# Optimization experiments

Hardware: AMD Instinct MI355X
Metric: run time of the kernel (lower is better)

Reference implementation:

```python
import jax, jax.numpy as jnp
import numpy as np

SIMPLE_W = 1.0
NON_SIMPLE_W = 5.0

# connectivity offset sets (exclude center)
_ALL26 = [(a, b, c) for a in (-1, 0, 1) for b in (-1, 0, 1) for c in (-1, 0, 1) if (a, b, c) != (0, 0, 0)]
OFF6 = [o for o in _ALL26 if abs(o[0]) + abs(o[1]) + abs(o[2]) == 1]          # scipy default structure
OFF18 = [o for o in _ALL26 if not (abs(o[0]) == 1 and abs(o[1]) == 1 and abs(o[2]) == 1)]  # the 's' structure
OFF26 = _ALL26                                                                  # np.ones((3,3,3))


def global_label(fg):
    """Connected-component labels (6-connectivity) via max-propagation.
    Labels are distinct positive ints per component (values differ from scipy's
    1..K but only label *equality* is used downstream). fg: bool [D,H,W]."""
    D, H, W = fg.shape
    idx = (jnp.arange(fg.size, dtype=jnp.int32) + 1).reshape(fg.shape)
    lab0 = jnp.where(fg, idx, 0)

    def step(lab):
        p = jnp.pad(lab, 1)
        m = lab
        for dz, dy, dx in OFF6:
            m = jnp.maximum(m, p[1 + dz:1 + dz + D, 1 + dy:1 + dy + H, 1 + dx:1 + dx + W])
        return jnp.where(fg, m, 0)

    def cond(c):
        return ~c[1]

    def body(c):
        lab, _ = c
        new = step(lab)
        return new, jnp.all(new == lab)

    lab, _ = jax.lax.while_loop(cond, body, (lab0, jnp.array(False)))
    return lab


def local_ncomp(mask, offsets):
    """Number of connected components inside each 3x3x3 window.
    mask: bool [N,3,3,3]. Max-propagation of unique seeds for 26 iters
    (>= max path length among 27 voxels); a component is counted where the
    surviving max label equals its own seed."""
    seed = (jnp.arange(27, dtype=jnp.int32) + 1).reshape(3, 3, 3)
    lab0 = jnp.where(mask, seed, 0)

    def body(_, lab):
        p = jnp.pad(lab, ((0, 0), (1, 1), (1, 1), (1, 1)))
        m = lab
        for dz, dy, dx in offsets:
            m = jnp.maximum(m, p[:, 1 + dz:4 + dz, 1 + dy:4 + dy, 1 + dx:4 + dx])
        return jnp.where(mask, m, 0)

    lab = jax.lax.fori_loop(0, 26, body, lab0)
    return jnp.sum((lab == seed) & mask, axis=(1, 2, 3))


def nonsimple_map(x):
    """Per-voxel non-simple-point indicator, float, same shape as x."""
    D, H, W = x.shape
    fg = x > 0
    glab = global_label(fg)
    p = jnp.pad(glab, 1, mode='edge')  # np.pad(..., 'edge')
    # 3x3x3 label windows per voxel -> [N,3,3,3]
    wins = jnp.stack([p[dz:dz + D, dy:dy + H, dx:dx + W]
                      for dz in range(3) for dy in range(3) for dx in range(3)], axis=-1)
    wins = wins.reshape(-1, 3, 3, 3)
    center = wins[:, 1, 1, 1]  # [N]
    c = center[:, None, None, None]
    # test 1: complement-of-center-label components (18-connectivity) must be exactly 1
    n1 = local_ncomp(wins != c, OFF18)
    # test 2: center-label components with center voxel removed (26-conn) must be exactly 1
    mask2 = (wins == c).at[:, 1, 1, 1].set(False)
    n2 = local_ncomp(mask2, OFF26)
    ns = (center != 0) & ((n1 != 1) | (n2 != 1))
    return ns.reshape(D, H, W).astype(x.dtype)


def setup_inputs() -> dict:
    key = jax.random.key(0)
    k1, k2 = jax.random.split(key)
    D = H = W = 64
    prediction = jax.random.normal(k1, (D, H, W), dtype=jnp.float32)
    label = jax.random.randint(k2, (D, H, W), 0, 2).astype(jnp.float32)
    return {"prediction": prediction, "label": label}


def reference(prediction, label):
    pw = nonsimple_map(prediction)
    lw = nonsimple_map(label)
    w_bool = (pw + lw) > 0
    weight = jnp.where(w_bool, NON_SIMPLE_W, SIMPLE_W).astype(prediction.dtype)
    # BCEWithLogitsLoss(reduction='none'): max(x,0) - x*y + log(1+exp(-|x|))
    cost = jnp.maximum(prediction, 0.0) - prediction * label + jnp.log1p(jnp.exp(-jnp.abs(prediction)))
    return jnp.mean(weight * cost)
```

## Files before the change

### kernel.cpp

```cpp
#include <hip/hip_runtime.h>

#define DIM 64
#define NVOX (DIM * DIM * DIM)

__device__ __forceinline__ int find_root_link(int* L, int v) {
    for (;;) {
        int p = L[v];
        if (p == v) return v;
        int gp = L[p];
        if (gp == p) return p;
        L[v] = gp;
        v = gp;
    }
}

__device__ __forceinline__ void unite(int* L, int a, int b) {
    int ra = find_root_link(L, a);
    int rb = find_root_link(L, b);
    while (ra != rb) {
        if (ra > rb) { int t = ra; ra = rb; rb = t; }
        int old = atomicCAS(&L[rb], rb, ra);
        if (old == rb) break;
        rb = find_root_link(L, old);
        ra = find_root_link(L, ra);
    }
}

__global__ void local_ccl(const float* __restrict__ pred,
                          const float* __restrict__ lab,
                          int* __restrict__ LP, int* __restrict__ LL) {
    __shared__ int s_lab[2048];
    int t = threadIdx.x;
    int b = blockIdx.x;
    int tx = b & 3, ty = (b >> 2) & 3, tz = b >> 4;
    int X0 = tx << 4, Y0 = ty << 4, Z0 = tz << 3;

    const float* src = blockIdx.y ? lab : pred;
    int* Lg = blockIdx.y ? LL : LP;

    bool fg[8];
    int vv[8];
#pragma unroll
    for (int i = 0; i < 8; ++i) {
        int l = t + (i << 8);
        int v = ((Z0 + (l >> 8)) << 12) | ((Y0 + ((l >> 4) & 15)) << 6)
              | (X0 + (l & 15));
        vv[i] = v;
        fg[i] = src[v] > 0.0f;
        s_lab[l] = fg[i] ? l : -1;
    }
    __syncthreads();

#pragma unroll
    for (int i = 0; i < 8; ++i) {
        if (!fg[i]) continue;
        int l = t + (i << 8);
        int lx = l & 15, ly = (l >> 4) & 15, lz = l >> 8;
        if (lx < 15 && s_lab[l + 1]   >= 0) unite(s_lab, l, l + 1);
        if (ly < 15 && s_lab[l + 16]  >= 0) unite(s_lab, l, l + 16);
        if (lz < 7  && s_lab[l + 256] >= 0) unite(s_lab, l, l + 256);
    }
    __syncthreads();

#pragma unroll
    for (int i = 0; i < 8; ++i) {
        int g = -1;
        if (fg[i]) {
            int p = s_lab[t + (i << 8)];
            while (s_lab[p] != p) p = s_lab[p];
            g = ((Z0 + (p >> 8)) << 12) | ((Y0 + ((p >> 4) & 15)) << 6)
              | (X0 + (p & 15));
        }
        Lg[vv[i]] = g;
    }
}

#define EPF 53248

__global__ void boundary_link(int* __restrict__ LP, int* __restrict__ LL) {
    int e = blockIdx.x * blockDim.x + threadIdx.x;
    int f = e >= EPF;
    int r = f ? e - EPF : e;
    int* L = f ? LL : LP;
    int v, n;
    if (r < 12288) {
        int plane = 15 + ((r >> 12) << 4);
        int ij = r & 4095;
        v = ((ij >> 6) << 12) | ((ij & 63) << 6) | plane;
        n = v + 1;
    } else if (r < 24576) {
        int r2 = r - 12288;
        int plane = 15 + ((r2 >> 12) << 4);
        int ij = r2 & 4095;
        v = ((ij >> 6) << 12) | (plane << 6) | (ij & 63);
        n = v + 64;
    } else {
        int r3 = r - 24576;
        int plane = 7 + ((r3 >> 12) << 3);
        int ij = r3 & 4095;
        v = (plane << 12) | ((ij >> 6) << 6) | (ij & 63);
        n = v + 4096;
    }
    if (L[v] >= 0 && L[n] >= 0) unite(L, v, n);
}

#define MX_L 0x6DB6DB6u
#define MX_R 0x36DB6DBu
#define MY_L 0x7E3F1F8u
#define MY_R 0x0FC7E3Fu
#define M27  0x7FFFFFFu

__device__ __forceinline__ unsigned dil26(unsigned m) {
    m |= ((m << 1) & MX_L) | ((m >> 1) & MX_R);
    m |= ((m << 3) & MY_L) | ((m >> 3) & MY_R);
    m |= ((m << 9) & M27)  | (m >> 9);
    return m;
}
__device__ __forceinline__ unsigned dil18(unsigned m) {
    unsigned ax = m | ((m << 1) & MX_L) | ((m >> 1) & MX_R);
    unsigned ay = m | ((m << 3) & MY_L) | ((m >> 3) & MY_R);
    unsigned dxy = ax | ((ax << 3) & MY_L) | ((ax >> 3) & MY_R);
    unsigned dxz = ax | ((ax << 9) & M27)  | (ax >> 9);
    unsigned dyz = ay | ((ay << 9) & M27)  | (ay >> 9);
    return dxy | dxz | dyz;
}

__device__ __forceinline__ bool single18(unsigned m) {
    if (!m) return false;
    unsigned c = m & (~m + 1u);
    for (;;) {
        unsigned n = dil18(c) & m;
        if (n == m) return true;
        if (n == c) return false;
        c = n;
    }
}
__device__ __forceinline__ bool single26(unsigned m) {
    if (!m) return false;
    unsigned c = m & (~m + 1u);
    for (;;) {
        unsigned n = dil26(c) & m;
        if (n == m) return true;
        if (n == c) return false;
        c = n;
    }
}

#define HV 600

__global__ void finalize_kernel(const float* __restrict__ pred,
                                const float* __restrict__ lab,
                                const int* __restrict__ LP,
                                const int* __restrict__ LL,
                                float* __restrict__ out) {
    __shared__ int sP[HV], sL[HV];
    __shared__ float s_part[4];
    int t = threadIdx.x;
    int b = blockIdx.x;
    int tx = b & 7, ty = (b >> 3) & 7, tz = b >> 6;
    int x0 = tx << 3, y0 = ty << 3, z0 = tz << 2;

    for (int i = t; i < HV; i += 256) {
        int hx = i % 10, r = i / 10, hy = r % 10, hz = r / 10;
        int gx = x0 + hx - 1; gx = gx < 0 ? 0 : (gx > 63 ? 63 : gx);
        int gy = y0 + hy - 1; gy = gy < 0 ? 0 : (gy > 63 ? 63 : gy);
        int gz = z0 + hz - 1; gz = gz < 0 ? 0 : (gz > 63 ? 63 : gz);
        int gv = (gz << 12) | (gy << 6) | gx;
        int p = LP[gv];
        if (p >= 0) { int q = LP[p]; while (q != p) { p = q; q = LP[p]; } }
        sP[i] = p;
        p = LL[gv];
        if (p >= 0) { int q = LL[p]; while (q != p) { p = q; q = LL[p]; } }
        sL[i] = p;
    }
    __syncthreads();

    int lx = t & 7, ly = (t >> 3) & 7, lz = t >> 6;
    int x = x0 | lx, y = y0 | ly, z = z0 | lz;
    int v = (z << 12) | (y << 6) | x;
    int base = lz * 100 + ly * 10 + lx;

    bool nsP = false, nsL = false;
    {
        int c = sP[base + 111];
        if (c >= 0) {
            unsigned m1 = 0, m2 = 0; int k = 0;
#pragma unroll
            for (int kz = 0; kz < 3; ++kz)
#pragma unroll
                for (int ky = 0; ky < 3; ++ky)
#pragma unroll
                    for (int kx = 0; kx < 3; ++kx, ++k) {
                        int w = sP[base + kz * 100 + ky * 10 + kx];
                        m1 |= (unsigned)(w != c) << k;
                        m2 |= (unsigned)(w == c) << k;
                    }
            m2 &= ~(1u << 13);
            nsP = !(single18(m1) && single26(m2));
        }
    }
    {
        int c = sL[base + 111];
        if (c >= 0) {
            unsigned m1 = 0, m2 = 0; int k = 0;
#pragma unroll
            for (int kz = 0; kz < 3; ++kz)
#pragma unroll
                for (int ky = 0; ky < 3; ++ky)
#pragma unroll
                    for (int kx = 0; kx < 3; ++kx, ++k) {
                        int w = sL[base + kz * 100 + ky * 10 + kx];
                        m1 |= (unsigned)(w != c) << k;
                        m2 |= (unsigned)(w == c) << k;
                    }
            m2 &= ~(1u << 13);
            nsL = !(single18(m1) && single26(m2));
        }
    }

    float p = pred[v], l = lab[v];
    float cost = fmaxf(p, 0.0f) - p * l + log1pf(__expf(-fabsf(p)));
    float w = (nsP || nsL) ? 5.0f : 1.0f;
    float contrib = w * cost;

#pragma unroll
    for (int off = 32; off > 0; off >>= 1)
        contrib += __shfl_down(contrib, off, 64);
    if ((t & 63) == 0) s_part[t >> 6] = contrib;
    __syncthreads();
    if (t == 0) {
        float s = s_part[0] + s_part[1] + s_part[2] + s_part[3];
        atomicAdd(out, s * (1.0f / (float)NVOX));
    }
}

extern "C" void kernel_launch(void* const* d_in, const int* in_sizes, int n_in,
                              void* d_out, int out_size, void* d_ws, size_t ws_size,
                              hipStream_t stream) {
    const float* pred = (const float*)d_in[0];
    const float* lab  = (const float*)d_in[1];
    float* out = (float*)d_out;

    int* LP = (int*)d_ws;
    int* LL = LP + NVOX;

    hipMemsetAsync(d_out, 0, sizeof(float), stream);

    hipLaunchKernelGGL(local_ccl, dim3(128, 2), dim3(256), 0, stream,
                       pred, lab, LP, LL);
    hipLaunchKernelGGL(boundary_link, dim3(2 * EPF / 256), dim3(256), 0, stream,
                       LP, LL);
    hipLaunchKernelGGL(finalize_kernel, dim3(NVOX / 256), dim3(256), 0, stream,
                       pred, lab, LP, LL, out);
}
```

Measured before the change: 116.0 us.

## Fuse CCL, boundary linking and finalize into one cooperative kernel

Merges the three kernel launches and the memset into a single cooperative kernel of 256 blocks, separating the local labeling, boundary union and finalize phases with grid-wide syncs. The finalize phase now gives each block a larger 16x8x8 tile, with each thread handling four voxels, which reduces halo overhead and the number of atomic adds. The intent is to remove launch and inter-kernel gaps for this small workload. In exchange it pays the cost of grid.sync and has less parallelism in the finalize phase.

Result: slower. 180.3 us (+55.4%).

```diff
diff --git a/kernel.cpp b/kernel.cpp
--- a/kernel.cpp
+++ b/kernel.cpp
@@ -1,7 +1,11 @@
 #include <hip/hip_runtime.h>
+#include <hip/hip_cooperative_groups.h>
+
+namespace cg = cooperative_groups;
 
 #define DIM 64
 #define NVOX (DIM * DIM * DIM)
+#define EPF 53248
 
 __device__ __forceinline__ int find_root_link(int* L, int v) {
     for (;;) {
@@ -26,84 +30,6 @@
     }
 }
 
-__global__ void local_ccl(const float* __restrict__ pred,
-                          const float* __restrict__ lab,
-                          int* __restrict__ LP, int* __restrict__ LL) {
-    __shared__ int s_lab[2048];
-    int t = threadIdx.x;
-    int b = blockIdx.x;
-    int tx = b & 3, ty = (b >> 2) & 3, tz = b >> 4;
-    int X0 = tx << 4, Y0 = ty << 4, Z0 = tz << 3;
-
-    const float* src = blockIdx.y ? lab : pred;
-    int* Lg = blockIdx.y ? LL : LP;
-
-    bool fg[8];
-    int vv[8];
-#pragma unroll
-    for (int i = 0; i < 8; ++i) {
-        int l = t + (i << 8);
-        int v = ((Z0 + (l >> 8)) << 12) | ((Y0 + ((l >> 4) & 15)) << 6)
-              | (X0 + (l & 15));
-        vv[i] = v;
-        fg[i] = src[v] > 0.0f;
-        s_lab[l] = fg[i] ? l : -1;
-    }
-    __syncthreads();
-
-#pragma unroll
-    for (int i = 0; i < 8; ++i) {
-        if (!fg[i]) continue;
-        int l = t + (i << 8);
-        int lx = l & 15, ly = (l >> 4) & 15, lz = l >> 8;
-        if (lx < 15 && s_lab[l + 1]   >= 0) unite(s_lab, l, l + 1);
-        if (ly < 15 && s_lab[l + 16]  >= 0) unite(s_lab, l, l + 16);
-        if (lz < 7  && s_lab[l + 256] >= 0) unite(s_lab, l, l + 256);
-    }
-    __syncthreads();
-
-#pragma unroll
-    for (int i = 0; i < 8; ++i) {
-        int g = -1;
-        if (fg[i]) {
-            int p = s_lab[t + (i << 8)];
-            while (s_lab[p] != p) p = s_lab[p];
-            g = ((Z0 + (p >> 8)) << 12) | ((Y0 + ((p >> 4) & 15)) << 6)
-              | (X0 + (p & 15));
-        }
-        Lg[vv[i]] = g;
-    }
-}
-
-#define EPF 53248
-
-__global__ void boundary_link(int* __restrict__ LP, int* __restrict__ LL) {
-    int e = blockIdx.x * blockDim.x + threadIdx.x;
-    int f = e >= EPF;
-    int r = f ? e - EPF : e;
-    int* L = f ? LL : LP;
-    int v, n;
-    if (r < 12288) {
-        int plane = 15 + ((r >> 12) << 4);
-        int ij = r & 4095;
-        v = ((ij >> 6) << 12) | ((ij & 63) << 6) | plane;
-        n = v + 1;
-    } else if (r < 24576) {
-        int r2 = r - 12288;
-        int plane = 15 + ((r2 >> 12) << 4);
-        int ij = r2 & 4095;
-        v = ((ij >> 6) << 12) | (plane << 6) | (ij & 63);
-        n = v + 64;
-    } else {
-        int r3 = r - 24576;
-        int plane = 7 + ((r3 >> 12) << 3);
-        int ij = r3 & 4095;
-        v = (plane << 12) | ((ij >> 6) << 6) | (ij & 63);
-        n = v + 4096;
-    }
-    if (L[v] >= 0 && L[n] >= 0) unite(L, v, n);
-}
-
 #define MX_L 0x6DB6DB6u
 #define MX_R 0x36DB6DBu
 #define MY_L 0x7E3F1F8u
@@ -146,91 +72,154 @@
     }
 }
 
-#define HV 600
-
-__global__ void finalize_kernel(const float* __restrict__ pred,
-                                const float* __restrict__ lab,
-                                const int* __restrict__ LP,
-                                const int* __restrict__ LL,
-                                float* __restrict__ out) {
-    __shared__ int sP[HV], sL[HV];
+__device__ __forceinline__ bool nonsimple(const int* __restrict__ s, int base) {
+    int c = s[base + 199];
+    if (c < 0) return false;
+    unsigned m1 = 0, m2 = 0; int k = 0;
+#pragma unroll
+    for (int kz = 0; kz < 3; ++kz)
+#pragma unroll
+        for (int ky = 0; ky < 3; ++ky)
+#pragma unroll
+            for (int kx = 0; kx < 3; ++kx, ++k) {
+                int w = s[base + kz * 180 + ky * 18 + kx];
+                m1 |= (unsigned)(w != c) << k;
+                m2 |= (unsigned)(w == c) << k;
+            }
+    m2 &= ~(1u << 13);
+    return !(single18(m1) && single26(m2));
+}
+
+__global__ void __launch_bounds__(256)
+fused_kernel(const float* __restrict__ pred, const float* __restrict__ lab,
+             int* __restrict__ LP, int* __restrict__ LL,
+             float* __restrict__ out) {
+    __shared__ int s_lab[2048];
+    __shared__ int sP[1800], sL[1800];
     __shared__ float s_part[4];
+    cg::grid_group grid = cg::this_grid();
     int t = threadIdx.x;
     int b = blockIdx.x;
-    int tx = b & 7, ty = (b >> 3) & 7, tz = b >> 6;
-    int x0 = tx << 3, y0 = ty << 3, z0 = tz << 2;
-
-    for (int i = t; i < HV; i += 256) {
-        int hx = i % 10, r = i / 10, hy = r % 10, hz = r / 10;
-        int gx = x0 + hx - 1; gx = gx < 0 ? 0 : (gx > 63 ? 63 : gx);
-        int gy = y0 + hy - 1; gy = gy < 0 ? 0 : (gy > 63 ? 63 : gy);
-        int gz = z0 + hz - 1; gz = gz < 0 ? 0 : (gz > 63 ? 63 : gz);
-        int gv = (gz << 12) | (gy << 6) | gx;
-        int p = LP[gv];
-        if (p >= 0) { int q = LP[p]; while (q != p) { p = q; q = LP[p]; } }
-        sP[i] = p;
-        p = LL[gv];
-        if (p >= 0) { int q = LL[p]; while (q != p) { p = q; q = LL[p]; } }
-        sL[i] = p;
-    }
-    __syncthreads();
-
-    int lx = t & 7, ly = (t >> 3) & 7, lz = t >> 6;
-    int x = x0 | lx, y = y0 | ly, z = z0 | lz;
-    int v = (z << 12) | (y << 6) | x;
-    int base = lz * 100 + ly * 10 + lx;
-
-    bool nsP = false, nsL = false;
+
     {
-        int c = sP[base + 111];
-        if (c >= 0) {
-            unsigned m1 = 0, m2 = 0; int k = 0;
-#pragma unroll
-            for (int kz = 0; kz < 3; ++kz)
-#pragma unroll
-                for (int ky = 0; ky < 3; ++ky)
-#pragma unroll
-                    for (int kx = 0; kx < 3; ++kx, ++k) {
-                        int w = sP[base + kz * 100 + ky * 10 + kx];
-                        m1 |= (unsigned)(w != c) << k;
-                        m2 |= (unsigned)(w == c) << k;
-                    }
-            m2 &= ~(1u << 13);
-            nsP = !(single18(m1) && single26(m2));
-        }
-    }
+        int f = b >> 7, m = b & 127;
+        int tx = m & 3, ty = (m >> 2) & 3, tz = m >> 4;
+        int X0 = tx << 4, Y0 = ty << 4, Z0 = tz << 3;
+        const float* src = f ? lab : pred;
+        int* Lg = f ? LL : LP;
+
+        bool fg[8];
+        int vv[8];
+#pragma unroll
+        for (int i = 0; i < 8; ++i) {
+            int l = t + (i << 8);
+            int v = ((Z0 + (l >> 8)) << 12) | ((Y0 + ((l >> 4) & 15)) << 6)
+                  | (X0 + (l & 15));
+            vv[i] = v;
+            fg[i] = src[v] > 0.0f;
+            s_lab[l] = fg[i] ? l : -1;
+        }
+        __syncthreads();
+
+#pragma unroll
+        for (int i = 0; i < 8; ++i) {
+            if (!fg[i]) continue;
+            int l = t + (i << 8);
+            int lx = l & 15, ly = (l >> 4) & 15, lz = l >> 8;
+            if (lx < 15 && s_lab[l + 1]   >= 0) unite(s_lab, l, l + 1);
+            if (ly < 15 && s_lab[l + 16]  >= 0) unite(s_lab, l, l + 16);
+            if (lz < 7  && s_lab[l + 256] >= 0) unite(s_lab, l, l + 256);
+        }
+        __syncthreads();
+
+#pragma unroll
+        for (int i = 0; i < 8; ++i) {
+            int g = -1;
+            if (fg[i]) {
+                int p = s_lab[t + (i << 8)];
+                while (s_lab[p] != p) p = s_lab[p];
+                g = ((Z0 + (p >> 8)) << 12) | ((Y0 + ((p >> 4) & 15)) << 6)
+                  | (X0 + (p & 15));
+            }
+            Lg[vv[i]] = g;
+        }
+    }
+    if (b == 0 && t == 0) *out = 0.0f;
+    grid.sync();
+
     {
-        int c = sL[base + 111];
-        if (c >= 0) {
-            unsigned m1 = 0, m2 = 0; int k = 0;
-#pragma unroll
-            for (int kz = 0; kz < 3; ++kz)
-#pragma unroll
-                for (int ky = 0; ky < 3; ++ky)
-#pragma unroll
-                    for (int kx = 0; kx < 3; ++kx, ++k) {
-                        int w = sL[base + kz * 100 + ky * 10 + kx];
-                        m1 |= (unsigned)(w != c) << k;
-                        m2 |= (unsigned)(w == c) << k;
-                    }
-            m2 &= ~(1u << 13);
-            nsL = !(single18(m1) && single26(m2));
-        }
-    }
-
-    float p = pred[v], l = lab[v];
-    float cost = fmaxf(p, 0.0f) - p * l + log1pf(__expf(-fabsf(p)));
-    float w = (nsP || nsL) ? 5.0f : 1.0f;
-    float contrib = w * cost;
-
-#pragma unroll
-    for (int off = 32; off > 0; off >>= 1)
-        contrib += __shfl_down(contrib, off, 64);
-    if ((t & 63) == 0) s_part[t >> 6] = contrib;
-    __syncthreads();
-    if (t == 0) {
-        float s = s_part[0] + s_part[1] + s_part[2] + s_part[3];
-        atomicAdd(out, s * (1.0f / (float)NVOX));
+        int tid = (b << 8) | t;
+        for (int e = tid; e < 2 * EPF; e += 65536) {
+            int f = e >= EPF;
+            int r = f ? e - EPF : e;
+            int* L = f ? LL : LP;
+            int v, n;
+            if (r < 12288) {
+                int plane = 15 + ((r >> 12) << 4);
+                int ij = r & 4095;
+                v = ((ij >> 6) << 12) | ((ij & 63) << 6) | plane;
+                n = v + 1;
+            } else if (r < 24576) {
+                int r2 = r - 12288;
+                int plane = 15 + ((r2 >> 12) << 4);
+                int ij = r2 & 4095;
+                v = ((ij >> 6) << 12) | (plane << 6) | (ij & 63);
+                n = v + 64;
+            } else {
+                int r3 = r - 24576;
+                int plane = 7 + ((r3 >> 12) << 3);
+                int ij = r3 & 4095;
+                v = (plane << 12) | ((ij >> 6) << 6) | (ij & 63);
+                n = v + 4096;
+            }
+            if (L[v] >= 0 && L[n] >= 0) unite(L, v, n);
+        }
+    }
+    grid.sync();
+
+    {
+        int rx = b & 3, ry = (b >> 2) & 7, rz = b >> 5;
+        int x0 = rx << 4, y0 = ry << 3, z0 = rz << 3;
+
+        for (int i = t; i < 1800; i += 256) {
+            int hx = i % 18, r = i / 18, hy = r % 10, hz = r / 10;
+            int gx = x0 + hx - 1; gx = gx < 0 ? 0 : (gx > 63 ? 63 : gx);
+            int gy = y0 + hy - 1; gy = gy < 0 ? 0 : (gy > 63 ? 63 : gy);
+            int gz = z0 + hz - 1; gz = gz < 0 ? 0 : (gz > 63 ? 63 : gz);
+            int gv = (gz << 12) | (gy << 6) | gx;
+            int p = LP[gv];
+            if (p >= 0) { int q = LP[p]; while (q != p) { p = q; q = LP[p]; } }
+            sP[i] = p;
+            p = LL[gv];
+            if (p >= 0) { int q = LL[p]; while (q != p) { p = q; q = LL[p]; } }
+            sL[i] = p;
+        }
+        __syncthreads();
+
+        float acc = 0.0f;
+#pragma unroll
+        for (int j = 0; j < 4; ++j) {
+            int l = t + (j << 8);
+            int lx = l & 15, ly = (l >> 4) & 7, lz = l >> 7;
+            int x = x0 | lx, y = y0 | ly, z = z0 | lz;
+            int v = (z << 12) | (y << 6) | x;
+            int base = lz * 180 + ly * 18 + lx;
+
+            bool ns = nonsimple(sP, base) || nonsimple(sL, base);
+            float p = pred[v], lv = lab[v];
+            float cost = fmaxf(p, 0.0f) - p * lv + log1pf(__expf(-fabsf(p)));
+            acc += (ns ? 5.0f : 1.0f) * cost;
+        }
+
+#pragma unroll
+        for (int off = 32; off > 0; off >>= 1)
+            acc += __shfl_down(acc, off, 64);
+        if ((t & 63) == 0) s_part[t >> 6] = acc;
+        __syncthreads();
+        if (t == 0) {
+            float s = s_part[0] + s_part[1] + s_part[2] + s_part[3];
+            atomicAdd(out, s * (1.0f / (float)NVOX));
+        }
     }
 }
 
@@ -240,16 +229,10 @@
     const float* pred = (const float*)d_in[0];
     const float* lab  = (const float*)d_in[1];
     float* out = (float*)d_out;
-
     int* LP = (int*)d_ws;
     int* LL = LP + NVOX;
 
-    hipMemsetAsync(d_out, 0, sizeof(float), stream);
-
-    hipLaunchKernelGGL(local_ccl, dim3(128, 2), dim3(256), 0, stream,
-                       pred, lab, LP, LL);
-    hipLaunchKernelGGL(boundary_link, dim3(2 * EPF / 256), dim3(256), 0, stream,
-                       LP, LL);
-    hipLaunchKernelGGL(finalize_kernel, dim3(NVOX / 256), dim3(256), 0, stream,
-                       pred, lab, LP, LL, out);
-}
+    void* args[] = { (void*)&pred, (void*)&lab, (void*)&LP, (void*)&LL, (void*)&out };
+    hipLaunchCooperativeKernel((const void*)fused_kernel, dim3(256), dim3(256),
+                               args, 0, stream);
+}
```

## Fold memset into CCL kernel and dedupe boundary unions per wavefront

Applied to the files above, without the earlier changes.

Removes the separate memset launch by zeroing the output inside the first CCL block. Boundary linking now handles both volumes in one thread over half as many threads, resolves roots before uniting, and skips a union when the neighbouring lane already has the same root pair. This is meant to cut launch overhead and atomic contention on shared roots. It relies on the finalize kernel running after local_ccl in the same stream, so ordering holds.

Result: no change. 114.1 us (-1.7%).

```diff
diff --git a/kernel.cpp b/kernel.cpp
--- a/kernel.cpp
+++ b/kernel.cpp
@@ -2,6 +2,7 @@
 
 #define DIM 64
 #define NVOX (DIM * DIM * DIM)
+#define EPF 53248
 
 __device__ __forceinline__ int find_root_link(int* L, int v) {
     for (;;) {
@@ -26,11 +27,19 @@
     }
 }
 
+__device__ __forceinline__ int chase(const int* __restrict__ L, int p) {
+    int q = L[p];
+    while (q != p) { p = q; q = L[p]; }
+    return p;
+}
+
 __global__ void local_ccl(const float* __restrict__ pred,
                           const float* __restrict__ lab,
-                          int* __restrict__ LP, int* __restrict__ LL) {
+                          int* __restrict__ LP, int* __restrict__ LL,
+                          float* __restrict__ out) {
     __shared__ int s_lab[2048];
     int t = threadIdx.x;
+    if (blockIdx.x == 0 && blockIdx.y == 0 && t == 0) *out = 0.0f;
     int b = blockIdx.x;
     int tx = b & 3, ty = (b >> 2) & 3, tz = b >> 4;
     int X0 = tx << 4, Y0 = ty << 4, Z0 = tz << 3;
@@ -75,13 +84,8 @@
     }
 }
 
-#define EPF 53248
-
 __global__ void boundary_link(int* __restrict__ LP, int* __restrict__ LL) {
-    int e = blockIdx.x * blockDim.x + threadIdx.x;
-    int f = e >= EPF;
-    int r = f ? e - EPF : e;
-    int* L = f ? LL : LP;
+    int r = blockIdx.x * blockDim.x + threadIdx.x;
     int v, n;
     if (r < 12288) {
         int plane = 15 + ((r >> 12) << 4);
@@ -101,7 +105,30 @@
         v = (plane << 12) | ((ij >> 6) << 6) | (ij & 63);
         n = v + 4096;
     }
-    if (L[v] >= 0 && L[n] >= 0) unite(L, v, n);
+
+    int pa = LP[v], pb = LP[n];
+    int la = LL[v], lb = LL[n];
+    bool doP = (pa >= 0) & (pb >= 0);
+    bool doL = (la >= 0) & (lb >= 0);
+
+    int rp0 = -1, rp1 = -1, rl0 = -1, rl1 = -1;
+    if (doP) {
+        int x0 = chase(LP, pa), x1 = chase(LP, pb);
+        rp0 = min(x0, x1); rp1 = max(x0, x1);
+    }
+    if (doL) {
+        int x0 = chase(LL, la), x1 = chase(LL, lb);
+        rl0 = min(x0, x1); rl1 = max(x0, x1);
+    }
+
+    int lane = threadIdx.x & 63;
+    int qp0 = __shfl_up(rp0, 1, 64), qp1 = __shfl_up(rp1, 1, 64);
+    int ql0 = __shfl_up(rl0, 1, 64), ql1 = __shfl_up(rl1, 1, 64);
+    bool dupP = lane && (qp0 == rp0) && (qp1 == rp1);
+    bool dupL = lane && (ql0 == rl0) && (ql1 == rl1);
+
+    if (doP && !dupP && rp0 != rp1) unite(LP, rp0, rp1);
+    if (doL && !dupL && rl0 != rl1) unite(LL, rl0, rl1);
 }
 
 #define MX_L 0x6DB6DB6u
@@ -167,10 +194,10 @@
         int gz = z0 + hz - 1; gz = gz < 0 ? 0 : (gz > 63 ? 63 : gz);
         int gv = (gz << 12) | (gy << 6) | gx;
         int p = LP[gv];
-        if (p >= 0) { int q = LP[p]; while (q != p) { p = q; q = LP[p]; } }
+        if (p >= 0) p = chase(LP, p);
         sP[i] = p;
         p = LL[gv];
-        if (p >= 0) { int q = LL[p]; while (q != p) { p = q; q = LL[p]; } }
+        if (p >= 0) p = chase(LL, p);
         sL[i] = p;
     }
     __syncthreads();
@@ -244,11 +271,9 @@
     int* LP = (int*)d_ws;
     int* LL = LP + NVOX;
 
-    hipMemsetAsync(d_out, 0, sizeof(float), stream);
-
     hipLaunchKernelGGL(local_ccl, dim3(128, 2), dim3(256), 0, stream,
-                       pred, lab, LP, LL);
-    hipLaunchKernelGGL(boundary_link, dim3(2 * EPF / 256), dim3(256), 0, stream,
+                       pred, lab, LP, LL, out);
+    hipLaunchKernelGGL(boundary_link, dim3(EPF / 256), dim3(256), 0, stream,
                        LP, LL);
     hipLaunchKernelGGL(finalize_kernel, dim3(NVOX / 256), dim3(256), 0, stream,
                        pred, lab, LP, LL, out);
```

## Fuse boundary union into local CCL kernel via per-face arrival handshake

Applied to the files above, without the earlier changes.

Merges the boundary-linking pass into the local labeling kernel. Each block marks its shared faces with an atomic exchange, and the second block to arrive at a face merges labels across it. Adjacent duplicate root pairs are filtered within a wavefront before calling unite. The output memset is folded into the kernel, which cuts the launch count from four to two. The face counters are never reset between calls, so on repeated runs a block may process a face before its neighbour has finished, creating a race.

Measured after the change: 152.6 us. 31.5% more time.

```diff
diff --git a/kernel.cpp b/kernel.cpp
--- a/kernel.cpp
+++ b/kernel.cpp
@@ -2,6 +2,8 @@
 
 #define DIM 64
 #define NVOX (DIM * DIM * DIM)
+#define NFACES 304
+#define MAGIC  0x5A5A5A5A
 
 __device__ __forceinline__ int find_root_link(int* L, int v) {
     for (;;) {
@@ -26,17 +28,26 @@
     }
 }
 
-__global__ void local_ccl(const float* __restrict__ pred,
-                          const float* __restrict__ lab,
-                          int* __restrict__ LP, int* __restrict__ LL) {
+__device__ __forceinline__ int chase(const int* __restrict__ L, int p) {
+    int q = L[p];
+    while (q != p) { p = q; q = L[p]; }
+    return p;
+}
+
+__global__ void __launch_bounds__(256)
+local_link(const float* __restrict__ pred, const float* __restrict__ lab,
+           int* __restrict__ LP, int* __restrict__ LL,
+           int* __restrict__ fctr, float* __restrict__ out) {
     __shared__ int s_lab[2048];
+    __shared__ int s_face[6];
     int t = threadIdx.x;
-    int b = blockIdx.x;
+    int b = blockIdx.x, f = blockIdx.y;
+    if (b == 0 && f == 0 && t == 0) *out = 0.0f;
+
     int tx = b & 3, ty = (b >> 2) & 3, tz = b >> 4;
     int X0 = tx << 4, Y0 = ty << 4, Z0 = tz << 3;
-
-    const float* src = blockIdx.y ? lab : pred;
-    int* Lg = blockIdx.y ? LL : LP;
+    const float* src = f ? lab : pred;
+    int* Lg = f ? LL : LP;
 
     bool fg[8];
     int vv[8];
@@ -73,35 +84,69 @@
         }
         Lg[vv[i]] = g;
     }
-}
-
-#define EPF 53248
-
-__global__ void boundary_link(int* __restrict__ LP, int* __restrict__ LL) {
-    int e = blockIdx.x * blockDim.x + threadIdx.x;
-    int f = e >= EPF;
-    int r = f ? e - EPF : e;
-    int* L = f ? LL : LP;
-    int v, n;
-    if (r < 12288) {
-        int plane = 15 + ((r >> 12) << 4);
-        int ij = r & 4095;
-        v = ((ij >> 6) << 12) | ((ij & 63) << 6) | plane;
-        n = v + 1;
-    } else if (r < 24576) {
-        int r2 = r - 12288;
-        int plane = 15 + ((r2 >> 12) << 4);
-        int ij = r2 & 4095;
-        v = ((ij >> 6) << 12) | (plane << 6) | (ij & 63);
-        n = v + 64;
-    } else {
-        int r3 = r - 24576;
-        int plane = 7 + ((r3 >> 12) << 3);
-        int ij = r3 & 4095;
-        v = (plane << 12) | ((ij >> 6) << 6) | (ij & 63);
-        n = v + 4096;
-    }
-    if (L[v] >= 0 && L[n] >= 0) unite(L, v, n);
+    __syncthreads();
+    __threadfence();
+
+    if (t < 6) {
+        int face = -1;
+        if      (t == 0 && tx > 0) face = (tz * 4 + ty) * 3 + (tx - 1);
+        else if (t == 1 && tx < 3) face = (tz * 4 + ty) * 3 + tx;
+        else if (t == 2 && ty > 0) face = 96 + (tz * 4 + tx) * 3 + (ty - 1);
+        else if (t == 3 && ty < 3) face = 96 + (tz * 4 + tx) * 3 + ty;
+        else if (t == 4 && tz > 0) face = 192 + (ty * 4 + tx) * 7 + (tz - 1);
+        else if (t == 5 && tz < 7) face = 192 + (ty * 4 + tx) * 7 + tz;
+        int proc = -1;
+        if (face >= 0) {
+            int old = atomicExch(&fctr[f * NFACES + face], MAGIC);
+            if (old == MAGIC) proc = face;
+        }
+        s_face[t] = proc;
+    }
+    __syncthreads();
+    __threadfence();
+
+    for (int s = 0; s < 6; ++s) {
+        int face = s_face[s];
+        if (face < 0) continue;
+        int v = -1, n = -1;
+        if (face < 96) {
+            if (t < 128) {
+                int txm = face % 3, r = face / 3;
+                int y = ((r & 3) << 4) | (t & 15);
+                int z = ((r >> 2) << 3) | (t >> 4);
+                v = (z << 12) | (y << 6) | ((txm << 4) | 15);
+                n = v + 1;
+            }
+        } else if (face < 192) {
+            if (t < 128) {
+                int g2 = face - 96;
+                int tym = g2 % 3, r = g2 / 3;
+                int x = ((r & 3) << 4) | (t & 15);
+                int z = ((r >> 2) << 3) | (t >> 4);
+                v = (z << 12) | (((tym << 4) | 15) << 6) | x;
+                n = v + 64;
+            }
+        } else {
+            int g2 = face - 192;
+            int tzm = g2 % 7, r = g2 / 7;
+            int x = ((r & 3) << 4) | (t & 15);
+            int y = ((r >> 2) << 4) | ((t >> 4) & 15);
+            v = (((tzm << 3) | 7) << 12) | (y << 6) | x;
+            n = v + 4096;
+        }
+        int r0 = -1, r1 = -1;
+        if (v >= 0) {
+            int a = Lg[v], c = Lg[n];
+            if (a >= 0 && c >= 0) {
+                int u0 = chase(Lg, a), u1 = chase(Lg, c);
+                r0 = min(u0, u1); r1 = max(u0, u1);
+            }
+        }
+        int lane = t & 63;
+        int q0 = __shfl_up(r0, 1, 64), q1 = __shfl_up(r1, 1, 64);
+        bool dup = lane && (q0 == r0) && (q1 == r1);
+        if (r0 >= 0 && r0 != r1 && !dup) unite(Lg, r0, r1);
+    }
 }
 
 #define MX_L 0x6DB6DB6u
@@ -167,10 +212,10 @@
         int gz = z0 + hz - 1; gz = gz < 0 ? 0 : (gz > 63 ? 63 : gz);
         int gv = (gz << 12) | (gy << 6) | gx;
         int p = LP[gv];
-        if (p >= 0) { int q = LP[p]; while (q != p) { p = q; q = LP[p]; } }
+        if (p >= 0) p = chase(LP, p);
         sP[i] = p;
         p = LL[gv];
-        if (p >= 0) { int q = LL[p]; while (q != p) { p = q; q = LL[p]; } }
+        if (p >= 0) p = chase(LL, p);
         sL[i] = p;
     }
     __syncthreads();
@@ -241,15 +286,12 @@
     const float* lab  = (const float*)d_in[1];
     float* out = (float*)d_out;
 
-    int* LP = (int*)d_ws;
-    int* LL = LP + NVOX;
-
-    hipMemsetAsync(d_out, 0, sizeof(float), stream);
-
-    hipLaunchKernelGGL(local_ccl, dim3(128, 2), dim3(256), 0, stream,
-                       pred, lab, LP, LL);
-    hipLaunchKernelGGL(boundary_link, dim3(2 * EPF / 256), dim3(256), 0, stream,
-                       LP, LL);
+    int* LP   = (int*)d_ws;
+    int* LL   = LP + NVOX;
+    int* fctr = LL + NVOX;
+
+    hipLaunchKernelGGL(local_link, dim3(128, 2), dim3(256), 0, stream,
+                       pred, lab, LP, LL, fctr, out);
     hipLaunchKernelGGL(finalize_kernel, dim3(NVOX / 256), dim3(256), 0, stream,
                        pred, lab, LP, LL, out);
 }
```
